# Performance work log

Hardware: AMD Instinct MI355X
Metric: run time of the kernel (lower is better)

## Reference

```python
import jax, jax.numpy as jnp
import numpy as np
import math

B, S, D, H, F = 4, 1024, 1024, 16, 4096
NUM_BUCKETS, MAX_DISTANCE = 32, 128
LN_EPS = 1e-5


def _relative_position_bucket(relative_position, num_buckets=NUM_BUCKETS, max_distance=MAX_DISTANCE):
    # bidirectional T5 bucketing, faithful to the torch source
    n = -relative_position
    num_buckets = num_buckets // 2  # 16
    ret = (n < 0).astype(jnp.int32) * num_buckets
    n = jnp.abs(n)
    max_exact = num_buckets // 2  # 8
    is_small = n < max_exact
    val_if_large = max_exact + (
        jnp.log(jnp.maximum(n, 1).astype(jnp.float32) / max_exact)
        / math.log(max_distance / max_exact)
        * (num_buckets - max_exact)
    ).astype(jnp.int32)
    val_if_large = jnp.minimum(val_if_large, num_buckets - 1)
    return ret + jnp.where(is_small, n, val_if_large)


def layer_norm(x, g, b):
    mu = jnp.mean(x, axis=-1, keepdims=True)
    var = jnp.mean((x - mu) ** 2, axis=-1, keepdims=True)
    return g * (x - mu) / jnp.sqrt(var + LN_EPS) + b


def setup_inputs() -> dict:
    key = jax.random.key(0)
    ks = jax.random.split(key, 12)
    s = 0.02
    return {
        "in_state": jax.random.normal(ks[0], (B, S, D), jnp.float32),
        "padding_mask": jnp.ones((B, S), jnp.int32),
        "Wq": jax.random.normal(ks[1], (D, D), jnp.float32) * s,
        "bq": jnp.zeros((D,), jnp.float32),
        "Wk": jax.random.normal(ks[2], (D, D), jnp.float32) * s,
        "bk": jnp.zeros((D,), jnp.float32),
        "Wv": jax.random.normal(ks[3], (D, D), jnp.float32) * s,
        "bv": jnp.zeros((D,), jnp.float32),
        "Wo": jax.random.normal(ks[4], (D, D), jnp.float32) * s,
        "bo": jnp.zeros((D,), jnp.float32),
        "rel_bias": jax.random.normal(ks[5], (NUM_BUCKETS, H), jnp.float32) * s,
        "ln1_g": jnp.ones((D,), jnp.float32),
        "ln1_b": jnp.zeros((D,), jnp.float32),
        "W1": jax.random.normal(ks[6], (D, F), jnp.float32) * s,
        "b1": jnp.zeros((F,), jnp.float32),
        "W2": jax.random.normal(ks[7], (F, D), jnp.float32) * s,
        "b2": jnp.zeros((D,), jnp.float32),
        "ln2_g": jnp.ones((D,), jnp.float32),
        "ln2_b": jnp.zeros((D,), jnp.float32),
    }


def reference(in_state, padding_mask, Wq, bq, Wk, bk, Wv, bv, Wo, bo, rel_bias,
              ln1_g, ln1_b, W1, b1, W2, b2, ln2_g, ln2_b):
    b, s, d = in_state.shape
    dh = d // H
    q = in_state @ Wq + bq
    k = in_state @ Wk + bk
    v = in_state @ Wv + bv
    # faithful to torch's q.view(B*H, S, d_head) flat reshape (no head transpose)
    qh = q.reshape(b * H, s, dh)
    kh = k.reshape(b * H, s, dh)
    vh = v.reshape(b * H, s, dh)
    scores = jnp.einsum('bqd,bkd->bqk', qh, kh)  # no 1/sqrt(d) scaling (T5 style)
    # relative position bias: [H, S, S] tiled over batch -> block index b*H+h gets head h
    rel_pos = jnp.arange(s)[:, None] - jnp.arange(s)[None, :]
    buckets = _relative_position_bucket(rel_pos)
    bias = rel_bias[buckets].transpose(2, 0, 1)  # [H, S, S]
    bias = jnp.tile(bias, (b, 1, 1))  # [B*H, S, S]
    # padding mask: log(0/1) -> -inf/0; block b*H+h uses mask[b, value_index]
    pad = jnp.log(padding_mask.astype(jnp.float32))  # [B, S]
    pad = jnp.repeat(pad, H, axis=0)[:, None, :]  # [B*H, 1, S]
    attw = jax.nn.softmax(scores + bias + pad, axis=-1)
    att = (attw @ vh).reshape(b, s, d)
    att = att @ Wo + bo
    h = layer_norm(att + in_state, ln1_g, ln1_b)
    ff = jnp.maximum(h @ W1 + b1, 0.0) @ W2 + b2
    out = layer_norm(ff + h, ln2_g, ln2_b)
    return out
```

## Files before the change

### kernel.cpp

```cpp
#include <hip/hip_runtime.h>
#include <hip/hip_bf16.h>

typedef unsigned short u16;
typedef __attribute__((ext_vector_type(8))) short bhalf8;
typedef __attribute__((ext_vector_type(4))) float f32x4;

#define DEV __device__ __forceinline__

DEV float bf2f(u16 u) { union { unsigned int i; float f; } c; c.i = ((unsigned int)u) << 16; return c.f; }
DEV u16 f2bf(float f) {
  union { float f; unsigned int i; } c; c.f = f;
  unsigned int x = c.i;
  x += 0x7fffu + ((x >> 16) & 1u);
  return (u16)(x >> 16);
}

DEV void async16(const void* g, void* l) {
  __builtin_amdgcn_global_load_lds((__attribute__((address_space(1))) void*)g,
                                   (__attribute__((address_space(3))) void*)l, 16, 0, 0);
}

struct Ptr11 { const void* p[11]; };
struct TC4 { const void* in[4]; u16* out[4]; };

__global__ void detect_kernel(const unsigned int* __restrict__ x, int* __restrict__ flag) {
  int t = threadIdx.x;
  int cnt = 0;
  for (int i = t; i < 256; i += 64) {
    unsigned int w = x[i];
    int e = (w >> 7) & 0xFF;
    if (e >= 96 && e <= 134) cnt++;
  }
#pragma unroll
  for (int o = 1; o < 64; o <<= 1) cnt += __shfl_xor(cnt, o, 64);
  if (t == 0) *flag = (cnt >= 192) ? 1 : 0;
}

DEV bhalf8 load8B(const void* base, size_t e, int isbf) {
  if (isbf) return *(const bhalf8*)((const u16*)base + e);
  const float* f = (const float*)base + e;
  float4 a = *(const float4*)f;
  float4 b = *(const float4*)(f + 4);
  bhalf8 r;
  r[0] = (short)f2bf(a.x); r[1] = (short)f2bf(a.y); r[2] = (short)f2bf(a.z); r[3] = (short)f2bf(a.w);
  r[4] = (short)f2bf(b.x); r[5] = (short)f2bf(b.y); r[6] = (short)f2bf(b.z); r[7] = (short)f2bf(b.w);
  return r;
}

__global__ __launch_bounds__(256) void convert_x(const void* __restrict__ x,
                                                 u16* __restrict__ dst,
                                                 const int* __restrict__ flag) {
  int c = blockIdx.x * 256 + threadIdx.x;
  u16* d = dst + (size_t)c * 4;
  if (*flag) {
    *(ushort4*)d = ((const ushort4*)x)[c];
  } else {
    float4 v = ((const float4*)x)[c];
    d[0] = f2bf(v.x); d[1] = f2bf(v.y); d[2] = f2bf(v.z); d[3] = f2bf(v.w);
  }
}

__global__ __launch_bounds__(256) void convert_small(Ptr11 s, float* __restrict__ dst,
                                                     const int* __restrict__ flag) {
  const int isbf = *flag;
  const int SZ[11] = {1024,1024,1024,1024,512,1024,1024,4096,1024,1024,1024};
  for (int i = threadIdx.x; i < 13824; i += 256) {
    int acc = 0, seg = -1, off = 0;
#pragma unroll
    for (int s2 = 0; s2 < 11; ++s2) {
      if (seg < 0 && i < acc + SZ[s2]) { seg = s2; off = i - acc; }
      acc += SZ[s2];
    }
    dst[i] = isbf ? bf2f(((const u16*)s.p[seg])[off]) : ((const float*)s.p[seg])[off];
  }
}

DEV void tconv_tile(const void* in, u16* out, int R, int C, int isbf) {
  __shared__ __align__(16) u16 tile[64][72];
  const int t = threadIdx.x;
  const int c0 = blockIdx.x * 64, r0 = blockIdx.y * 64;
#pragma unroll
  for (int r = 0; r < 2; ++r) {
    int idx = r * 256 + t;
    int ri = idx >> 3, cc = (idx & 7) * 8;
    bhalf8 v = load8B(in, (size_t)(r0 + ri) * C + c0 + cc, isbf);
    *(bhalf8*)(&tile[ri][cc]) = v;
  }
  __syncthreads();
#pragma unroll
  for (int r = 0; r < 2; ++r) {
    int idx = r * 256 + t;
    int co = idx >> 3, rc = (idx & 7) * 8;
    bhalf8 v;
#pragma unroll
    for (int ii = 0; ii < 8; ++ii) v[ii] = (short)tile[rc + ii][co];
    *(bhalf8*)(out + (size_t)(c0 + co) * R + r0 + rc) = v;
  }
}

__global__ __launch_bounds__(256) void tconv_w4(TC4 p, const int* __restrict__ flag) {
  int z = blockIdx.z;
  tconv_tile(p.in[z], p.out[z], 1024, 1024, *flag);
}

__global__ __launch_bounds__(256) void tconv_generic(const void* in, u16* out, int R, int C,
                                                     const int* __restrict__ flag) {
  tconv_tile(in, out, R, C, *flag);
}

__global__ __launch_bounds__(256) void transpose_generic(const u16* in, u16* out, int R, int C) {
  __shared__ __align__(16) u16 tile[64][72];
  const int t = threadIdx.x;
  const int c0 = blockIdx.x * 64, r0 = blockIdx.y * 64;
  size_t bs = (size_t)R * C * blockIdx.z;
#pragma unroll
  for (int r = 0; r < 2; ++r) {
    int idx = r * 256 + t;
    int ri = idx >> 3, cc = (idx & 7) * 8;
    *(bhalf8*)(&tile[ri][cc]) = *(const bhalf8*)(in + bs + (size_t)(r0 + ri) * C + c0 + cc);
  }
  __syncthreads();
#pragma unroll
  for (int r = 0; r < 2; ++r) {
    int idx = r * 256 + t;
    int co = idx >> 3, rc = (idx & 7) * 8;
    bhalf8 v;
#pragma unroll
    for (int ii = 0; ii < 8; ++ii) v[ii] = (short)tile[rc + ii][co];
    *(bhalf8*)(out + bs + (size_t)(c0 + co) * R + r0 + rc) = v;
  }
}

template<int RELU>
__global__ __launch_bounds__(512) void gemm_bt(
    const u16* __restrict__ A, const u16* __restrict__ BT0,
    const float* __restrict__ b0, const float* __restrict__ b1, const float* __restrict__ b2,
    u16* __restrict__ C0, int M, int N, int K, long sBT, long sC)
{
  __shared__ __align__(16) u16 ldsA[128 * 32];
  __shared__ __align__(16) u16 ldsB[128 * 32];

  const int t = threadIdx.x;
  const int wv = t >> 6, l = t & 63;
  const int wm = wv >> 2, wn = wv & 3;
  const int m0 = blockIdx.y * 128, n0 = blockIdx.x * 128;
  const int z = blockIdx.z;

  const u16* BT = BT0 + (long)z * sBT;
  const float* bias = (z == 0) ? b0 : (z == 1 ? b1 : b2);
  u16* C = C0 + (long)z * sC;

  const int mm_s = t >> 2, kc_s = (t & 3) ^ ((t >> 4) & 3);
  const u16* agp = A + (size_t)(m0 + mm_s) * K + kc_s * 8;
  const u16* bgp = BT + (size_t)(n0 + mm_s) * K + kc_s * 8;
  char* la = (char*)ldsA + wv * 1024;
  char* lb = (char*)ldsB + wv * 1024;

  int a_off[4], b_off[2];
#pragma unroll
  for (int i = 0; i < 4; ++i) {
    int mm = wm * 64 + i * 16 + (l & 15);
    a_off[i] = (mm * 4 + ((l >> 4) ^ ((mm >> 2) & 3))) * 8;
  }
#pragma unroll
  for (int j = 0; j < 2; ++j) {
    int nn = wn * 32 + j * 16 + (l & 15);
    b_off[j] = (nn * 4 + ((l >> 4) ^ ((nn >> 2) & 3))) * 8;
  }

  f32x4 acc[4][2] = {};

  for (int kt = 0; kt < K; kt += 32) {
    __syncthreads();
    async16(agp + kt, la);
    async16(bgp + kt, lb);
    __syncthreads();

    bhalf8 af[4], bfr[2];
#pragma unroll
    for (int i = 0; i < 4; ++i) af[i] = *(const bhalf8*)(ldsA + a_off[i]);
#pragma unroll
    for (int j = 0; j < 2; ++j) bfr[j] = *(const bhalf8*)(ldsB + b_off[j]);
#pragma unroll
    for (int mi = 0; mi < 4; ++mi)
#pragma unroll
      for (int nj = 0; nj < 2; ++nj)
        acc[mi][nj] = __builtin_amdgcn_mfma_f32_16x16x32_bf16(af[mi], bfr[nj], acc[mi][nj], 0, 0, 0);
  }

  const int lr = (l >> 4) << 2, lc = l & 15;
#pragma unroll
  for (int nj = 0; nj < 2; ++nj) {
    int col = n0 + wn * 32 + nj * 16 + lc;
    float bb = bias[col];
#pragma unroll
    for (int mi = 0; mi < 4; ++mi) {
#pragma unroll
      for (int r = 0; r < 4; ++r) {
        int row = m0 + wm * 64 + mi * 16 + lr + r;
        float v = acc[mi][nj][r] + bb;
        if (RELU) v = fmaxf(v, 0.0f);
        C[(size_t)row * N + col] = f2bf(v);
      }
    }
  }
}

template<int RELU>
__global__ __launch_bounds__(256) void gemm_bn(
    const u16* __restrict__ A, const void* __restrict__ B,
    const float* __restrict__ bias, u16* __restrict__ C, int M, int N, int K,
    const int* __restrict__ flag)
{
  __shared__ __align__(16) u16 ldsA[128][40];
  __shared__ __align__(16) u16 ldsB[128][40];

  const int isbf = *flag;
  const int t = threadIdx.x;
  const int wv = t >> 6, l = t & 63;
  const int wm = wv & 1, wn = wv >> 1;
  const int m0 = blockIdx.y * 128, n0 = blockIdx.x * 128;

  const int srow = t >> 1, scol = (t & 1) * 16;
  const u16* agp = A + (size_t)(m0 + srow) * K + scol;

  const int kk = t >> 3;
  const int nn = (t & 7) * 16;

  f32x4 acc[4][4] = {};

  for (int kt = 0; kt < K; kt += 32) {
    bhalf8 a0 = *(const bhalf8*)(agp + kt);
    bhalf8 a1 = *(const bhalf8*)(agp + kt + 8);
    size_t e0 = (size_t)(kt + kk) * N + n0 + nn;
    bhalf8 b0v = load8B(B, e0, isbf);
    bhalf8 b1v = load8B(B, e0 + 8, isbf);
    __syncthreads();
    *(bhalf8*)(&ldsA[srow][scol])     = a0;
    *(bhalf8*)(&ldsA[srow][scol + 8]) = a1;
#pragma unroll
    for (int j = 0; j < 8; ++j) ldsB[nn + j][kk]     = (u16)b0v[j];
#pragma unroll
    for (int j = 0; j < 8; ++j) ldsB[nn + 8 + j][kk] = (u16)b1v[j];
    __syncthreads();

    bhalf8 af[4], bfr[4];
#pragma unroll
    for (int i = 0; i < 4; ++i)
      af[i] = *(const bhalf8*)(&ldsA[wm * 64 + i * 16 + (l & 15)][(l >> 4) * 8]);
#pragma unroll
    for (int i = 0; i < 4; ++i)
      bfr[i] = *(const bhalf8*)(&ldsB[wn * 64 + i * 16 + (l & 15)][(l >> 4) * 8]);
#pragma unroll
    for (int mi = 0; mi < 4; ++mi)
#pragma unroll
      for (int ni = 0; ni < 4; ++ni)
        acc[mi][ni] = __builtin_amdgcn_mfma_f32_16x16x32_bf16(af[mi], bfr[ni], acc[mi][ni], 0, 0, 0);
  }

  const int lr = (l >> 4) << 2, lc = l & 15;
#pragma unroll
  for (int ni = 0; ni < 4; ++ni) {
    int col = n0 + wn * 64 + ni * 16 + lc;
    float bb = bias[col];
#pragma unroll
    for (int mi = 0; mi < 4; ++mi) {
#pragma unroll
      for (int r = 0; r < 4; ++r) {
        int row = m0 + wm * 64 + mi * 16 + lr + r;
        float v = acc[mi][ni][r] + bb;
        if (RELU) v = fmaxf(v, 0.0f);
        C[(size_t)row * N + col] = f2bf(v);
      }
    }
  }
}

__global__ __launch_bounds__(256) void lut_kernel(const float* __restrict__ rbc, float* __restrict__ lut) {
  int idx = blockIdx.x * 256 + threadIdx.x;
  if (idx >= 16 * 2047) return;
  int h = idx / 2047;
  int dp = idx - h * 2047;
  int delta = dp - 1023;
  int n = -delta;
  int ret = 0;
  if (n < 0) { ret = 16; n = -n; }
  int bkt;
  if (n < 8) bkt = n;
  else {
    float v = logf((float)n * 0.125f) / logf(16.0f) * 8.0f;
    bkt = 8 + (int)v;
    if (bkt > 15) bkt = 15;
  }
  lut[idx] = (rbc[(ret + bkt) * 16 + h] - 12.0f) * 1.44269504f;
}

__global__ __launch_bounds__(256) void attn_fused(
    const u16* __restrict__ q, const u16* __restrict__ k, const u16* __restrict__ vt,
    const int* __restrict__ mask, const float* __restrict__ lut, u16* __restrict__ att)
{
  __shared__ __align__(16) u16 ldsQ[64][72];
  __shared__ __align__(16) u16 ldsK[64][72];
  __shared__ __align__(16) u16 ldsV[64][72];
  __shared__ __align__(16) u16 ldsP[4][16][72];
  __shared__ float ldsLut[2047];
  __shared__ float ldsPad[64];

  const int t = threadIdx.x;
  const int wv = t >> 6, l = t & 63;
  const int bh = blockIdx.x, qt = blockIdx.y;
  const int b = bh >> 4, h = bh & 15;
  const size_t base = (size_t)bh * 65536;
  const int q0 = qt * 64;

  for (int i = t; i < 2047; i += 256) ldsLut[i] = lut[h * 2047 + i];

  const int sr = t >> 2, sc = (t & 3) * 16;
  {
    bhalf8 q0v = *(const bhalf8*)(q + base + (size_t)(q0 + sr) * 64 + sc);
    bhalf8 q1v = *(const bhalf8*)(q + base + (size_t)(q0 + sr) * 64 + sc + 8);
    *(bhalf8*)(&ldsQ[sr][sc])     = q0v;
    *(bhalf8*)(&ldsQ[sr][sc + 8]) = q1v;
  }
  __syncthreads();

  bhalf8 qf[2];
  {
    int mm = wv * 16 + (l & 15);
#pragma unroll
    for (int s = 0; s < 2; ++s)
      qf[s] = *(const bhalf8*)(&ldsQ[mm][s * 32 + (l >> 4) * 8]);
  }

  float ls_part[4] = {0.0f, 0.0f, 0.0f, 0.0f};
  f32x4 acc_o[4] = {};

  const int* mrow = mask + b * 1024;

  for (int kt = 0; kt < 16; ++kt) {
    const int k0 = kt * 64;
    bhalf8 k0v = *(const bhalf8*)(k + base + (size_t)(k0 + sr) * 64 + sc);
    bhalf8 k1v = *(const bhalf8*)(k + base + (size_t)(k0 + sr) * 64 + sc + 8);
    bhalf8 v0v = *(const bhalf8*)(vt + base + (size_t)sr * 1024 + k0 + sc);
    bhalf8 v1v = *(const bhalf8*)(vt + base + (size_t)sr * 1024 + k0 + sc + 8);
    __syncthreads();
    *(bhalf8*)(&ldsK[sr][sc])     = k0v;
    *(bhalf8*)(&ldsK[sr][sc + 8]) = k1v;
    *(bhalf8*)(&ldsV[sr][sc])     = v0v;
    *(bhalf8*)(&ldsV[sr][sc + 8]) = v1v;
    if (t < 64) {
      int mv = mrow[k0 + t];
      ldsPad[t] = (mv > 0) ? __log2f((float)mv) : -1e30f;
    }
    __syncthreads();

    f32x4 accS[4] = {};
#pragma unroll
    for (int s = 0; s < 2; ++s) {
#pragma unroll
      for (int ni = 0; ni < 4; ++ni) {
        int nnj = ni * 16 + (l & 15);
        bhalf8 kf = *(const bhalf8*)(&ldsK[nnj][s * 32 + (l >> 4) * 8]);
        accS[ni] = __builtin_amdgcn_mfma_f32_16x16x32_bf16(qf[s], kf, accS[ni], 0, 0, 0);
      }
    }

    float padv[4];
#pragma unroll
    for (int ni = 0; ni < 4; ++ni) padv[ni] = ldsPad[ni * 16 + (l & 15)];
    const int ib = q0 + wv * 16 + ((l >> 4) << 2);
#pragma unroll
    for (int r = 0; r < 4; ++r) {
      int i_l = ((l >> 4) << 2) + r;
#pragma unroll
      for (int ni = 0; ni < 4; ++ni) {
        int j_l = ni * 16 + (l & 15);
        float s = fmaf(accS[ni][r], 1.44269504f, ldsLut[(ib + r) - (k0 + j_l) + 1023]) + padv[ni];
        float p = exp2f(s);
        ls_part[r] += p;
        ldsP[wv][i_l][j_l] = f2bf(p);
      }
    }

#pragma unroll
    for (int s = 0; s < 2; ++s) {
      int mm = l & 15;
      bhalf8 pf = *(const bhalf8*)(&ldsP[wv][mm][s * 32 + (l >> 4) * 8]);
#pragma unroll
      for (int ni = 0; ni < 4; ++ni) {
        int e = ni * 16 + (l & 15);
        bhalf8 vf = *(const bhalf8*)(&ldsV[e][s * 32 + (l >> 4) * 8]);
        acc_o[ni] = __builtin_amdgcn_mfma_f32_16x16x32_bf16(pf, vf, acc_o[ni], 0, 0, 0);
      }
    }
  }

#pragma unroll
  for (int r = 0; r < 4; ++r) {
#pragma unroll
    for (int off = 1; off < 16; off <<= 1) ls_part[r] += __shfl_xor(ls_part[r], off, 64);
    ls_part[r] = 1.0f / ls_part[r];
  }

#pragma unroll
  for (int ni = 0; ni < 4; ++ni) {
#pragma unroll
    for (int r = 0; r < 4; ++r) {
      int i = q0 + wv * 16 + ((l >> 4) << 2) + r;
      int e = ni * 16 + (l & 15);
      att[base + (size_t)i * 64 + e] = f2bf(acc_o[ni][r] * ls_part[r]);
    }
  }
}

template<int LAST>
__global__ __launch_bounds__(256) void ln_kernel(
    const u16* __restrict__ x, const u16* __restrict__ res,
    const float* __restrict__ g, const float* __restrict__ b,
    void* __restrict__ out, const int* __restrict__ flag)
{
  const int row = blockIdx.x, t = threadIdx.x;
  const size_t off = (size_t)row * 1024 + t * 4;
  ushort4 xv = *(const ushort4*)(x + off);
  ushort4 rv = *(const ushort4*)(res + off);
  float v0 = bf2f(xv.x) + bf2f(rv.x);
  float v1 = bf2f(xv.y) + bf2f(rv.y);
  float v2 = bf2f(xv.z) + bf2f(rv.z);
  float v3 = bf2f(xv.w) + bf2f(rv.w);
  float s = v0 + v1 + v2 + v3;
  float sq = v0 * v0 + v1 * v1 + v2 * v2 + v3 * v3;
#pragma unroll
  for (int o = 1; o < 64; o <<= 1) { s += __shfl_xor(s, o, 64); sq += __shfl_xor(sq, o, 64); }
  __shared__ float red[8];
  const int wv = t >> 6, l = t & 63;
  if (l == 0) { red[wv] = s; red[4 + wv] = sq; }
  __syncthreads();
  s = red[0] + red[1] + red[2] + red[3];
  sq = red[4] + red[5] + red[6] + red[7];
  float mu = s * 0.0009765625f;
  float var = sq * 0.0009765625f - mu * mu;
  float rstd = rsqrtf(var + 1e-5f);
  float4 gv = *(const float4*)(g + t * 4);
  float4 bv = *(const float4*)(b + t * 4);
  float o0 = gv.x * (v0 - mu) * rstd + bv.x;
  float o1 = gv.y * (v1 - mu) * rstd + bv.y;
  float o2 = gv.z * (v2 - mu) * rstd + bv.z;
  float o3 = gv.w * (v3 - mu) * rstd + bv.w;
  if (!LAST) {
    ushort4 ov; ov.x = f2bf(o0); ov.y = f2bf(o1); ov.z = f2bf(o2); ov.w = f2bf(o3);
    *(ushort4*)((u16*)out + off) = ov;
  } else {
    if (*flag) {
      ushort4 ov; ov.x = f2bf(o0); ov.y = f2bf(o1); ov.z = f2bf(o2); ov.w = f2bf(o3);
      *(ushort4*)((u16*)out + off) = ov;
    } else {
      float4 ov; ov.x = o0; ov.y = o1; ov.z = o2; ov.w = o3;
      *(float4*)((float*)out + off) = ov;
    }
  }
}

extern "C" void kernel_launch(void* const* d_in, const int* in_sizes, int n_in,
                              void* d_out, int out_size, void* d_ws, size_t ws_size,
                              hipStream_t stream) {
  const void* x  = d_in[0];
  const int* mask = (const int*)d_in[1];
  const void* Wq = d_in[2];  const void* bq = d_in[3];
  const void* Wk = d_in[4];  const void* bk = d_in[5];
  const void* Wv = d_in[6];  const void* bv = d_in[7];
  const void* Wo = d_in[8];  const void* bo = d_in[9];
  const void* rb = d_in[10];
  const void* g1 = d_in[11]; const void* be1 = d_in[12];
  const void* W1 = d_in[13]; const void* b1 = d_in[14];
  const void* W2 = d_in[15]; const void* b2 = d_in[16];
  const void* g2 = d_in[17]; const void* be2 = d_in[18];

  char* ws = (char*)d_ws;
  const size_t MB = 1024 * 1024;
  const bool FAST = (ws_size >= 57 * MB);

  const size_t TAIL = FAST ? 56 * MB : 48 * MB;
  float* smalls = (float*)(ws + TAIL);
  float* lut    = (float*)(ws + TAIL + 56 * 1024);
  int*   flag   = (int*)(ws + TAIL + 192 * 1024);

  float* bqc  = smalls + 0;
  float* bkc  = smalls + 1024;
  float* bvc  = smalls + 2048;
  float* boc  = smalls + 3072;
  float* rbc  = smalls + 4096;
  float* g1c  = smalls + 4608;
  float* be1c = smalls + 5632;
  float* b1c  = smalls + 6656;
  float* b2c  = smalls + 10752;
  float* g2c  = smalls + 11776;
  float* be2c = smalls + 12800;

  detect_kernel<<<1, 64, 0, stream>>>((const unsigned int*)x, flag);
  Ptr11 sml;
  sml.p[0] = bq; sml.p[1] = bk; sml.p[2] = bv; sml.p[3] = bo; sml.p[4] = rb;
  sml.p[5] = g1; sml.p[6] = be1; sml.p[7] = b1; sml.p[8] = b2; sml.p[9] = g2; sml.p[10] = be2;
  convert_small<<<1, 256, 0, stream>>>(sml, smalls, flag);
  lut_kernel<<<dim3(128), 256, 0, stream>>>(rbc, lut);

  if (FAST) {
    u16* xc   = (u16*)(ws + 0 * MB);
    u16* WqT  = (u16*)(ws + 8 * MB);
    u16* WkT  = WqT + 1048576;
    u16* WvT  = WqT + 2 * 1048576;
    u16* WoT  = WqT + 3 * 1048576;
    u16* qb   = (u16*)(ws + 16 * MB);
    u16* kb   = (u16*)(ws + 24 * MB);
    u16* vb   = (u16*)(ws + 32 * MB);
    u16* vtb  = (u16*)(ws + 40 * MB);
    u16* attb = (u16*)(ws + 32 * MB);
    u16* xo   = (u16*)(ws + 16 * MB);
    u16* hb   = (u16*)(ws + 48 * MB);
    u16* W1T  = (u16*)(ws + 8 * MB);
    u16* W2T  = (u16*)(ws + 0 * MB);
    u16* ff1  = (u16*)(ws + 16 * MB);
    u16* ff2o = (u16*)(ws + 8 * MB);

    convert_x<<<4096, 256, 0, stream>>>(x, xc, flag);
    TC4 tw; tw.in[0] = Wq; tw.in[1] = Wk; tw.in[2] = Wv; tw.in[3] = Wo;
    tw.out[0] = WqT; tw.out[1] = WkT; tw.out[2] = WvT; tw.out[3] = WoT;
    tconv_w4<<<dim3(16, 16, 4), 256, 0, stream>>>(tw, flag);

    gemm_bt<0><<<dim3(8, 32, 3), 512, 0, stream>>>(xc, WqT, bqc, bkc, bvc, qb,
                                                   4096, 1024, 1024, 1048576L, 4194304L);
    transpose_generic<<<dim3(1, 16, 64), 256, 0, stream>>>(vb, vtb, 1024, 64);
    attn_fused<<<dim3(64, 16), 256, 0, stream>>>(qb, kb, vtb, mask, lut, attb);
    gemm_bt<0><<<dim3(8, 32, 1), 512, 0, stream>>>(attb, WoT, boc, boc, boc, xo,
                                                   4096, 1024, 1024, 0L, 0L);
    tconv_generic<<<dim3(64, 16), 256, 0, stream>>>(W1, W1T, 1024, 4096, flag);
    ln_kernel<0><<<dim3(4096), 256, 0, stream>>>(xo, xc, g1c, be1c, hb, flag);
    tconv_generic<<<dim3(16, 64), 256, 0, stream>>>(W2, W2T, 4096, 1024, flag);
    gemm_bt<1><<<dim3(32, 32, 1), 512, 0, stream>>>(hb, W1T, b1c, b1c, b1c, ff1,
                                                    4096, 4096, 1024, 0L, 0L);
    gemm_bt<0><<<dim3(8, 32, 1), 512, 0, stream>>>(ff1, W2T, b2c, b2c, b2c, ff2o,
                                                   4096, 1024, 4096, 0L, 0L);
    ln_kernel<1><<<dim3(4096), 256, 0, stream>>>(ff2o, hb, g2c, be2c, d_out, flag);
  } else {
    u16* xc   = (u16*)(ws + 0 * MB);
    u16* WqT  = (u16*)(ws + 8 * MB);
    u16* WkT  = WqT + 1048576;
    u16* WvT  = WqT + 2 * 1048576;
    u16* WoT  = WqT + 3 * 1048576;
    u16* qb   = (u16*)(ws + 16 * MB);
    u16* kb   = (u16*)(ws + 24 * MB);
    u16* vb   = (u16*)(ws + 32 * MB);
    u16* vtb  = (u16*)(ws + 40 * MB);
    u16* attb = (u16*)(ws + 32 * MB);
    u16* xo   = (u16*)(ws + 16 * MB);
    u16* hb   = (u16*)(ws + 40 * MB);
    u16* ff1  = (u16*)(ws + 0 * MB);
    u16* ff2o = (u16*)(ws + 32 * MB);

    convert_x<<<4096, 256, 0, stream>>>(x, xc, flag);
    TC4 tw; tw.in[0] = Wq; tw.in[1] = Wk; tw.in[2] = Wv; tw.in[3] = Wo;
    tw.out[0] = WqT; tw.out[1] = WkT; tw.out[2] = WvT; tw.out[3] = WoT;
    tconv_w4<<<dim3(16, 16, 4), 256, 0, stream>>>(tw, flag);

    gemm_bt<0><<<dim3(8, 32, 3), 512, 0, stream>>>(xc, WqT, bqc, bkc, bvc, qb,
                                                   4096, 1024, 1024, 1048576L, 4194304L);
    transpose_generic<<<dim3(1, 16, 64), 256, 0, stream>>>(vb, vtb, 1024, 64);
    attn_fused<<<dim3(64, 16), 256, 0, stream>>>(qb, kb, vtb, mask, lut, attb);
    gemm_bt<0><<<dim3(8, 32, 1), 512, 0, stream>>>(attb, WoT, boc, boc, boc, xo,
                                                   4096, 1024, 1024, 0L, 0L);
    ln_kernel<0><<<dim3(4096), 256, 0, stream>>>(xo, xc, g1c, be1c, hb, flag);
    gemm_bn<1><<<dim3(32, 32), 256, 0, stream>>>(hb, W1, b1c, ff1, 4096, 4096, 1024, flag);
    gemm_bn<0><<<dim3(8, 32), 256, 0, stream>>>(ff1, W2, b2c, ff2o, 4096, 1024, 4096, flag);
    ln_kernel<1><<<dim3(4096), 256, 0, stream>>>(ff2o, hb, g2c, be2c, d_out, flag);
  }
}
```

Measured before the change: 433.4 us.

## Double-buffer LDS tiles in gemm_bt and merge LUT build into small-param prep

Result: no change. 440.0 us (+1.5%).

```diff
diff --git a/kernel.cpp b/kernel.cpp
--- a/kernel.cpp
+++ b/kernel.cpp
@@ -60,18 +60,40 @@
   }
 }
 
-__global__ __launch_bounds__(256) void convert_small(Ptr11 s, float* __restrict__ dst,
-                                                     const int* __restrict__ flag) {
+__global__ __launch_bounds__(256) void prep_small(Ptr11 s, float* __restrict__ dst,
+                                                  float* __restrict__ lut,
+                                                  const int* __restrict__ flag) {
+  __shared__ float rbl[512];
   const int isbf = *flag;
   const int SZ[11] = {1024,1024,1024,1024,512,1024,1024,4096,1024,1024,1024};
-  for (int i = threadIdx.x; i < 13824; i += 256) {
+  const int t = threadIdx.x;
+  for (int i = t; i < 13824; i += 256) {
     int acc = 0, seg = -1, off = 0;
 #pragma unroll
     for (int s2 = 0; s2 < 11; ++s2) {
       if (seg < 0 && i < acc + SZ[s2]) { seg = s2; off = i - acc; }
       acc += SZ[s2];
     }
-    dst[i] = isbf ? bf2f(((const u16*)s.p[seg])[off]) : ((const float*)s.p[seg])[off];
+    float v = isbf ? bf2f(((const u16*)s.p[seg])[off]) : ((const float*)s.p[seg])[off];
+    dst[i] = v;
+    if (i >= 4096 && i < 4608) rbl[i - 4096] = v;
+  }
+  __syncthreads();
+  for (int idx = t; idx < 16 * 2047; idx += 256) {
+    int h = idx / 2047;
+    int dp = idx - h * 2047;
+    int delta = dp - 1023;
+    int n = -delta;
+    int ret = 0;
+    if (n < 0) { ret = 16; n = -n; }
+    int bkt;
+    if (n < 8) bkt = n;
+    else {
+      float v = logf((float)n * 0.125f) / logf(16.0f) * 8.0f;
+      bkt = 8 + (int)v;
+      if (bkt > 15) bkt = 15;
+    }
+    lut[idx] = (rbl[(ret + bkt) * 16 + h] - 12.0f) * 1.44269504f;
   }
 }
 
@@ -137,8 +159,11 @@
     const float* __restrict__ b0, const float* __restrict__ b1, const float* __restrict__ b2,
     u16* __restrict__ C0, int M, int N, int K, long sBT, long sC)
 {
-  __shared__ __align__(16) u16 ldsA[128 * 32];
-  __shared__ __align__(16) u16 ldsB[128 * 32];
+  constexpr int WAIT_P = 0xF70 | 2;
+  constexpr int WAIT_0 = 0xF70;
+
+  __shared__ __align__(16) u16 ldsA[2][128 * 32];
+  __shared__ __align__(16) u16 ldsB[2][128 * 32];
 
   const int t = threadIdx.x;
   const int wv = t >> 6, l = t & 63;
@@ -153,8 +178,6 @@
   const int mm_s = t >> 2, kc_s = (t & 3) ^ ((t >> 4) & 3);
   const u16* agp = A + (size_t)(m0 + mm_s) * K + kc_s * 8;
   const u16* bgp = BT + (size_t)(n0 + mm_s) * K + kc_s * 8;
-  char* la = (char*)ldsA + wv * 1024;
-  char* lb = (char*)ldsB + wv * 1024;
 
   int a_off[4], b_off[2];
 #pragma unroll
@@ -169,18 +192,29 @@
   }
 
   f32x4 acc[4][2] = {};
-
-  for (int kt = 0; kt < K; kt += 32) {
-    __syncthreads();
-    async16(agp + kt, la);
-    async16(bgp + kt, lb);
-    __syncthreads();
+  const int nT = K >> 5;
+
+  async16(agp, (char*)(&ldsA[0][0]) + wv * 1024);
+  async16(bgp, (char*)(&ldsB[0][0]) + wv * 1024);
+
+  for (int kt = 0; kt < nT; ++kt) {
+    const int cur = kt & 1;
+    __builtin_amdgcn_s_barrier();
+    if (kt + 1 < nT) {
+      const int koff = (kt + 1) << 5;
+      async16(agp + koff, (char*)(&ldsA[cur ^ 1][0]) + wv * 1024);
+      async16(bgp + koff, (char*)(&ldsB[cur ^ 1][0]) + wv * 1024);
+      __builtin_amdgcn_s_waitcnt(WAIT_P);
+    } else {
+      __builtin_amdgcn_s_waitcnt(WAIT_0);
+    }
+    __builtin_amdgcn_s_barrier();
 
     bhalf8 af[4], bfr[2];
 #pragma unroll
-    for (int i = 0; i < 4; ++i) af[i] = *(const bhalf8*)(ldsA + a_off[i]);
-#pragma unroll
-    for (int j = 0; j < 2; ++j) bfr[j] = *(const bhalf8*)(ldsB + b_off[j]);
+    for (int i = 0; i < 4; ++i) af[i] = *(const bhalf8*)(&ldsA[cur][0] + a_off[i]);
+#pragma unroll
+    for (int j = 0; j < 2; ++j) bfr[j] = *(const bhalf8*)(&ldsB[cur][0] + b_off[j]);
 #pragma unroll
     for (int mi = 0; mi < 4; ++mi)
 #pragma unroll
@@ -274,25 +308,6 @@
       }
     }
   }
-}
-
-__global__ __launch_bounds__(256) void lut_kernel(const float* __restrict__ rbc, float* __restrict__ lut) {
-  int idx = blockIdx.x * 256 + threadIdx.x;
-  if (idx >= 16 * 2047) return;
-  int h = idx / 2047;
-  int dp = idx - h * 2047;
-  int delta = dp - 1023;
-  int n = -delta;
-  int ret = 0;
-  if (n < 0) { ret = 16; n = -n; }
-  int bkt;
-  if (n < 8) bkt = n;
-  else {
-    float v = logf((float)n * 0.125f) / logf(16.0f) * 8.0f;
-    bkt = 8 + (int)v;
-    if (bkt > 15) bkt = 15;
-  }
-  lut[idx] = (rbc[(ret + bkt) * 16 + h] - 12.0f) * 1.44269504f;
 }
 
 __global__ __launch_bounds__(256) void attn_fused(
@@ -488,7 +503,6 @@
   float* bkc  = smalls + 1024;
   float* bvc  = smalls + 2048;
   float* boc  = smalls + 3072;
-  float* rbc  = smalls + 4096;
   float* g1c  = smalls + 4608;
   float* be1c = smalls + 5632;
   float* b1c  = smalls + 6656;
@@ -500,8 +514,7 @@
   Ptr11 sml;
   sml.p[0] = bq; sml.p[1] = bk; sml.p[2] = bv; sml.p[3] = bo; sml.p[4] = rb;
   sml.p[5] = g1; sml.p[6] = be1; sml.p[7] = b1; sml.p[8] = b2; sml.p[9] = g2; sml.p[10] = be2;
-  convert_small<<<1, 256, 0, stream>>>(sml, smalls, flag);
-  lut_kernel<<<dim3(128), 256, 0, stream>>>(rbc, lut);
+  prep_small<<<1, 256, 0, stream>>>(sml, smalls, lut, flag);
 
   if (FAST) {
     u16* xc   = (u16*)(ws + 0 * MB);
```
